# Kernel tuning notes

Measured on AMD Instinct MI355X. Metric: run time of the kernel, lower is better.

Reference implementation:

```python
import jax, jax.numpy as jnp
import numpy as np

B, N, CTX, IMG_DIM = 8, 256, 196, 1024
DIM, NUM_TOKENS, DEPTH = 512, 10000, 6
D_STATE, D_CONV, HEADS = 16, 4, 8
D_INNER = 2 * DIM
DT_RANK = DIM // 16  # mamba-ssm default ceil(d_model/16)
HEAD_DIM = DIM // HEADS


def setup_inputs() -> dict:
    key = jax.random.key(0)
    ks = [jax.random.fold_in(key, i) for i in range(40)]
    it = iter(ks)
    def rn(shape, s=0.02):
        return jax.random.normal(next(it), shape, dtype=jnp.float32) * s
    inp = {}
    inp["text"] = jax.random.randint(next(it), (B, N), 0, NUM_TOKENS)
    inp["images"] = jax.random.normal(next(it), (B, CTX, IMG_DIM), dtype=jnp.float32)
    inp["dyt_alpha"] = jnp.float32(0.5)
    inp["dyt_gamma"] = jnp.ones((IMG_DIM,), jnp.float32)
    inp["dyt_beta"] = jnp.zeros((IMG_DIM,), jnp.float32)
    inp["img_W"] = rn((IMG_DIM, DIM))
    inp["img_b"] = jnp.zeros((DIM,), jnp.float32)
    inp["gate1_W"] = rn((DIM, DIM // 4))
    inp["gate1_b"] = jnp.zeros((DIM // 4,), jnp.float32)
    inp["gate2_W"] = rn((DIM // 4, DIM))
    inp["gate2_b"] = jnp.zeros((DIM,), jnp.float32)
    inp["token_emb"] = rn((NUM_TOKENS, DIM), 0.01)
    inp["pos_emb"] = rn((1024, DIM))
    inp["ln1_g"] = jnp.ones((DEPTH, DIM), jnp.float32)
    inp["ln1_b"] = jnp.zeros((DEPTH, DIM), jnp.float32)
    inp["in_proj_W"] = rn((DEPTH, DIM, 2 * D_INNER))
    inp["conv_W"] = rn((DEPTH, D_INNER, D_CONV), 0.1)
    inp["conv_b"] = jnp.zeros((DEPTH, D_INNER), jnp.float32)
    inp["x_proj_W"] = rn((DEPTH, D_INNER, DT_RANK + 2 * D_STATE))
    inp["dt_proj_W"] = rn((DEPTH, DT_RANK, D_INNER), 0.1)
    inp["dt_proj_b"] = jnp.full((DEPTH, D_INNER), -4.0, jnp.float32)
    inp["A_log"] = jnp.tile(jnp.log(jnp.arange(1, D_STATE + 1, dtype=jnp.float32))[None, None, :], (DEPTH, D_INNER, 1))
    inp["D_skip"] = jnp.ones((DEPTH, D_INNER), jnp.float32)
    inp["out_proj_W"] = rn((DEPTH, D_INNER, DIM))
    inp["ln2_g"] = jnp.ones((DEPTH, DIM), jnp.float32)
    inp["ln2_b"] = jnp.zeros((DEPTH, DIM), jnp.float32)
    inp["attn_in_W"] = rn((DEPTH, 3 * DIM, DIM))
    inp["attn_in_b"] = jnp.zeros((DEPTH, 3 * DIM), jnp.float32)
    inp["attn_out_W"] = rn((DEPTH, DIM, DIM))
    inp["attn_out_b"] = jnp.zeros((DEPTH, DIM), jnp.float32)
    inp["fnorm_g"] = jnp.ones((DIM,), jnp.float32)
    inp["fnorm_b"] = jnp.zeros((DIM,), jnp.float32)
    inp["logits_W"] = rn((DIM, NUM_TOKENS), 0.01)
    inp["logits_b"] = jnp.zeros((NUM_TOKENS,), jnp.float32)
    return inp


def _layernorm(x, g, b, eps=1e-5):
    m = x.mean(-1, keepdims=True)
    v = ((x - m) ** 2).mean(-1, keepdims=True)
    return (x - m) * jax.lax.rsqrt(v + eps) * g + b


def _silu(x):
    return x * jax.nn.sigmoid(x)


def _mamba(x, inW, cW, cb, xpW, dtW, dtb, A_log, D_skip, outW):
    # x: [b, n, DIM] -> [b, n, DIM]; selective scan (S6)
    b, n, _ = x.shape
    xz = x @ inW                                  # [b,n,2*di]
    xi, z = jnp.split(xz, 2, axis=-1)
    # causal depthwise conv1d, kernel D_CONV
    xp = jnp.pad(xi, ((0, 0), (D_CONV - 1, 0), (0, 0)))
    xc = sum(xp[:, k:k + n, :] * cW[:, k] for k in range(D_CONV)) + cb
    xc = _silu(xc)                                # [b,n,di]
    dbl = xc @ xpW                                # [b,n,dt_rank+2*ds]
    dt = jax.nn.softplus(dbl[..., :DT_RANK] @ dtW + dtb)      # [b,n,di]
    Bm = dbl[..., DT_RANK:DT_RANK + D_STATE]      # [b,n,ds]
    Cm = dbl[..., DT_RANK + D_STATE:]             # [b,n,ds]
    A = -jnp.exp(A_log)                           # [di,ds]
    dA = jnp.exp(dt[..., None] * A)               # [b,n,di,ds]
    dBx = dt[..., None] * Bm[:, :, None, :] * xc[..., None]   # [b,n,di,ds]
    def step(h, inputs):
        dA_t, dBx_t, C_t = inputs
        h = h * dA_t + dBx_t                      # [b,di,ds]
        y = jnp.einsum('bds,bs->bd', h, C_t)
        return h, y
    h0 = jnp.zeros((b, D_INNER, D_STATE), x.dtype)
    _, ys = jax.lax.scan(step, h0, (dA.transpose(1, 0, 2, 3), dBx.transpose(1, 0, 2, 3), Cm.transpose(1, 0, 2)))
    y = ys.transpose(1, 0, 2) + xc * D_skip       # [b,n,di]
    y = y * _silu(z)
    return y @ outW


def _cross_attn(q_in, kv, inW, inb, outW, outb):
    # torch nn.MultiheadAttention (batch_first) with packed in_proj
    Wq, Wk, Wv = jnp.split(inW, 3, axis=0)
    bq, bk, bv = jnp.split(inb, 3)
    def heads(t):
        return t.reshape(t.shape[0], t.shape[1], HEADS, HEAD_DIM).transpose(0, 2, 1, 3)
    q = heads(q_in @ Wq.T + bq)
    k = heads(kv @ Wk.T + bk)
    v = heads(kv @ Wv.T + bv)
    scale = HEAD_DIM ** -0.5
    att = jax.nn.softmax(jnp.einsum('bhqd,bhkd->bhqk', q * scale, k), axis=-1)
    o = jnp.einsum('bhqk,bhkd->bhqd', att, v).transpose(0, 2, 1, 3)
    o = o.reshape(q_in.shape)
    return o @ outW.T + outb


def _forward(text, images, dyt_alpha, dyt_gamma, dyt_beta, img_W, img_b,
             gate1_W, gate1_b, gate2_W, gate2_b, token_emb, pos_emb,
             ln1_g, ln1_b, in_proj_W, conv_W, conv_b, x_proj_W, dt_proj_W,
             dt_proj_b, A_log, D_skip, out_proj_W, ln2_g, ln2_b,
             attn_in_W, attn_in_b, attn_out_W, attn_out_b,
             fnorm_g, fnorm_b, logits_W, logits_b):
    # img_proj: DyT -> Linear (dropout = identity at eval)
    img = dyt_gamma * jnp.tanh(dyt_alpha * images) + dyt_beta
    img = img @ img_W + img_b                     # [b,ctx,dim]
    # MedicalAttentionGate: mean-pool over sequence -> channel gate
    att = img.mean(axis=1)                        # [b,dim]
    att = jax.nn.gelu(att @ gate1_W + gate1_b, approximate=False)
    att = jax.nn.sigmoid(att @ gate2_W + gate2_b)
    img = img * att[:, None, :]
    # decoder
    n = text.shape[1]
    x = token_emb[text] + pos_emb[:n]
    for l in range(DEPTH):
        xn = _layernorm(x, ln1_g[l], ln1_b[l])
        x = x + _mamba(xn, in_proj_W[l], conv_W[l], conv_b[l], x_proj_W[l],
                       dt_proj_W[l], dt_proj_b[l], A_log[l], D_skip[l], out_proj_W[l])
        xn = _layernorm(x, ln2_g[l], ln2_b[l])
        x = x + _cross_attn(xn, img, attn_in_W[l], attn_in_b[l], attn_out_W[l], attn_out_b[l])
    x = _layernorm(x, fnorm_g, fnorm_b)
    return x @ logits_W + logits_b                # [b,n,num_tokens]


def reference(text, images, dyt_alpha, dyt_gamma, dyt_beta, img_W, img_b,
              gate1_W, gate1_b, gate2_W, gate2_b, token_emb, pos_emb,
              ln1_g, ln1_b, in_proj_W, conv_W, conv_b, x_proj_W, dt_proj_W,
              dt_proj_b, A_log, D_skip, out_proj_W, ln2_g, ln2_b,
              attn_in_W, attn_in_b, attn_out_W, attn_out_b,
              fnorm_g, fnorm_b, logits_W, logits_b):
    return _forward(text, images, dyt_alpha, dyt_gamma, dyt_beta, img_W, img_b,
                    gate1_W, gate1_b, gate2_W, gate2_b, token_emb, pos_emb,
                    ln1_g, ln1_b, in_proj_W, conv_W, conv_b, x_proj_W, dt_proj_W,
                    dt_proj_b, A_log, D_skip, out_proj_W, ln2_g, ln2_b,
                    attn_in_W, attn_in_b, attn_out_W, attn_out_b,
                    fnorm_g, fnorm_b, logits_W, logits_b)
```

## Files before the change

kernel.cpp:

```cpp
#include <hip/hip_runtime.h>
#include <hip/hip_bf16.h>
#include <stdint.h>

#define B_    8
#define N_    256
#define CTX_  196
#define CTXP_ 224
#define CTXF_ 13
#define IMGD_ 1024
#define DIM_  512
#define DEPTH_ 6
#define DIN_  1024
#define DTR_  32
#define DST_  16
#define HEADS_ 8
#define HD_   64
#define NCHUNK_ 16
#define CLEN_   16
#define DG_     4

typedef __bf16 bf16x8 __attribute__((ext_vector_type(8)));
typedef __bf16 bf16x4 __attribute__((ext_vector_type(4)));
typedef float  f32x4  __attribute__((ext_vector_type(4)));

__device__ __forceinline__ float dpp_red16(float v) {
    int y;
    y = __builtin_amdgcn_update_dpp(0, __float_as_int(v), 0xB1, 0xF, 0xF, true);
    v += __int_as_float(y);
    y = __builtin_amdgcn_update_dpp(0, __float_as_int(v), 0x4E, 0xF, 0xF, true);
    v += __int_as_float(y);
    y = __builtin_amdgcn_update_dpp(0, __float_as_int(v), 0x141, 0xF, 0xF, true);
    v += __int_as_float(y);
    y = __builtin_amdgcn_update_dpp(0, __float_as_int(v), 0x140, 0xF, 0xF, true);
    v += __int_as_float(y);
    return v;
}
__device__ __forceinline__ float dpp_max16(float v) {
    int y;
    y = __builtin_amdgcn_update_dpp(0, __float_as_int(v), 0xB1, 0xF, 0xF, true);
    v = fmaxf(v, __int_as_float(y));
    y = __builtin_amdgcn_update_dpp(0, __float_as_int(v), 0x4E, 0xF, 0xF, true);
    v = fmaxf(v, __int_as_float(y));
    y = __builtin_amdgcn_update_dpp(0, __float_as_int(v), 0x141, 0xF, 0xF, true);
    v = fmaxf(v, __int_as_float(y));
    y = __builtin_amdgcn_update_dpp(0, __float_as_int(v), 0x140, 0xF, 0xF, true);
    v = fmaxf(v, __int_as_float(y));
    return v;
}

__device__ __forceinline__ void gload16(const void* g, void* l) {
    __builtin_amdgcn_global_load_lds(
        (const __attribute__((address_space(1))) uint32_t*)g,
        (__attribute__((address_space(3))) uint32_t*)l, 16, 0, 0);
}


__global__ void dyt_kernel(const float* __restrict__ img, const float* __restrict__ alpha_p,
                           const float* __restrict__ gamma, const float* __restrict__ beta,
                           __bf16* __restrict__ out, int total) {
    int i = blockIdx.x * 256 + threadIdx.x;
    if (i >= total) return;
    float a = alpha_p[0];
    int c = i & (IMGD_ - 1);
    out[i] = (__bf16)(gamma[c] * tanhf(a * img[i]) + beta[c]);
}

__global__ void pool_kernel(const float* __restrict__ imgf, float* __restrict__ pooled) {
    int i = blockIdx.x * 256 + threadIdx.x;
    if (i >= B_ * DIM_) return;
    int b = i >> 9, c = i & (DIM_ - 1);
    const float* p = imgf + (size_t)b * CTX_ * DIM_ + c;
    float s = 0.f;
    for (int t = 0; t < CTX_; ++t) s += p[t * DIM_];
    pooled[i] = s * (1.f / CTX_);
}

__global__ void gate1_kernel(const float* __restrict__ pooled, const float* __restrict__ W,
                             const float* __restrict__ bias, float* __restrict__ g1) {
    int i = blockIdx.x * 256 + threadIdx.x;
    if (i >= B_ * 128) return;
    int b = i >> 7, j = i & 127;
    const float* p = pooled + b * DIM_;
    float s = bias[j];
    for (int c = 0; c < DIM_; ++c) s += p[c] * W[c * 128 + j];
    g1[i] = 0.5f * s * (1.f + erff(s * 0.70710678118654752f));
}

__global__ void gate2_kernel(const float* __restrict__ g1, const float* __restrict__ W,
                             const float* __restrict__ bias, float* __restrict__ gate) {
    int i = blockIdx.x * 256 + threadIdx.x;
    if (i >= B_ * DIM_) return;
    int b = i >> 9, c = i & (DIM_ - 1);
    const float* p = g1 + b * 128;
    float s = bias[c];
    for (int j = 0; j < 128; ++j) s += p[j] * W[j * DIM_ + c];
    gate[i] = 1.f / (1.f + __expf(-s));
}

__global__ void scale_kernel(const float* __restrict__ imgf, const float* __restrict__ gate,
                             __bf16* __restrict__ imgfb) {
    int i = blockIdx.x * 256 + threadIdx.x;
    if (i >= B_ * CTX_ * DIM_) return;
    int c = i & (DIM_ - 1);
    int b = i / (CTX_ * DIM_);
    imgfb[i] = (__bf16)(imgf[i] * gate[b * DIM_ + c]);
}

__global__ void embed_kernel(const int* __restrict__ text, const float* __restrict__ temb,
                             const float* __restrict__ pemb, float* __restrict__ x) {
    int i = blockIdx.x * 256 + threadIdx.x;
    if (i >= B_ * N_ * DIM_) return;
    int c = i & (DIM_ - 1);
    int row = i >> 9;
    int n = row & (N_ - 1);
    int tok = text[row];
    x[i] = temb[(size_t)tok * DIM_ + c] + pemb[(size_t)n * DIM_ + c];
}

__global__ void ln_kernel(const float* __restrict__ x, const float* __restrict__ g,
                          const float* __restrict__ b, __bf16* __restrict__ o, int rows) {
    int row = blockIdx.x * 4 + (threadIdx.x >> 6);
    if (row >= rows) return;
    int lane = threadIdx.x & 63;
    const float* xr = x + (size_t)row * DIM_ + lane * 8;
    float4 v0 = ((const float4*)xr)[0];
    float4 v1 = ((const float4*)xr)[1];
    float r[8] = {v0.x, v0.y, v0.z, v0.w, v1.x, v1.y, v1.z, v1.w};
    float sum = 0.f, sq = 0.f;
    #pragma unroll
    for (int j = 0; j < 8; ++j) { sum += r[j]; sq += r[j] * r[j]; }
    #pragma unroll
    for (int m = 1; m < 64; m <<= 1) { sum += __shfl_xor(sum, m); sq += __shfl_xor(sq, m); }
    float mean = sum * (1.f / DIM_);
    float var  = sq * (1.f / DIM_) - mean * mean;
    float inv  = rsqrtf(fmaxf(var, 0.f) + 1e-5f);
    const float* gp = g + lane * 8;
    const float* bp = b + lane * 8;
    __bf16* op = o + (size_t)row * DIM_ + lane * 8;
    bf16x8 ov;
    #pragma unroll
    for (int j = 0; j < 8; ++j) ov[j] = (__bf16)((r[j] - mean) * inv * gp[j] + bp[j]);
    *(bf16x8*)op = ov;
}

__global__ void conv_silu_kernel(const __bf16* __restrict__ xzb, const float* __restrict__ cw,
                                 const float* __restrict__ cb, __bf16* __restrict__ xcb) {
    int idx = blockIdx.x * 256 + threadIdx.x;
    if (idx >= B_ * N_ * DIN_ / 4) return;
    int i4 = idx * 4;
    int d = i4 & (DIN_ - 1);
    int row = i4 >> 10;
    int n = row & (N_ - 1);
    int rowb = row - n;
    float4 acc = *(const float4*)(cb + d);
    #pragma unroll
    for (int k = 0; k < 4; ++k) {
        int m = n - 3 + k;
        if (m >= 0) {
            bf16x4 v = *(const bf16x4*)(xzb + (size_t)(rowb + m) * (2 * DIN_) + d);
            acc.x += (float)v[0] * cw[(d + 0) * 4 + k];
            acc.y += (float)v[1] * cw[(d + 1) * 4 + k];
            acc.z += (float)v[2] * cw[(d + 2) * 4 + k];
            acc.w += (float)v[3] * cw[(d + 3) * 4 + k];
        }
    }
    bf16x4 p;
    p[0] = (__bf16)(acc.x / (1.f + __expf(-acc.x)));
    p[1] = (__bf16)(acc.y / (1.f + __expf(-acc.y)));
    p[2] = (__bf16)(acc.z / (1.f + __expf(-acc.z)));
    p[3] = (__bf16)(acc.w / (1.f + __expf(-acc.w)));
    *(bf16x4*)(xcb + i4) = p;
}

__global__ void cvt_bf16_kernel(const float* __restrict__ src, __bf16* __restrict__ dst, int count) {
    int i = (blockIdx.x * 256 + threadIdx.x) * 4;
    if (i >= count) return;
    float4 v = *(const float4*)(src + i);
    bf16x4 p = {(__bf16)v.x, (__bf16)v.y, (__bf16)v.z, (__bf16)v.w};
    *(bf16x4*)(dst + i) = p;
}

__global__ void cvt_rows_kernel(const float* __restrict__ src, __bf16* __restrict__ dst,
                                int totalRows, int rpl, int off) {
    int t = blockIdx.x * 256 + threadIdx.x;
    int total = totalRows * (DIM_ / 4);
    if (t >= total) return;
    int i = t / (DIM_ / 4), c4 = (t % (DIM_ / 4)) * 4;
    int l = i / rpl, r = i % rpl;
    const float* s = src + ((size_t)l * 1536 + off + r) * DIM_ + c4;
    float4 v = *(const float4*)s;
    bf16x4 p = {(__bf16)v.x, (__bf16)v.y, (__bf16)v.z, (__bf16)v.w};
    *(bf16x4*)(dst + (size_t)i * DIM_ + c4) = p;
}

__global__ __launch_bounds__(256) void scanf_kernel(
    const __bf16* __restrict__ xcb, const float* __restrict__ dbl,
    const __bf16* __restrict__ xzb, const float* __restrict__ dtw,
    const float* __restrict__ dtb, const float* __restrict__ A_log,
    const float* __restrict__ Dsk, __bf16* __restrict__ ybb) {
    __shared__ float sdt[DG_][N_], su[DG_][N_];
    __shared__ float sA[DG_][256], sB[DG_][256];
    int bid = blockIdx.x;
    int nwg = gridDim.x;
    int bd = (bid & 7) * (nwg >> 3) + (bid >> 3);
    int dg = bd & (DIN_ / DG_ - 1), b = bd / (DIN_ / DG_);
    int d0 = dg * DG_;
    int tid = threadIdx.x, s = tid & 15, c = tid >> 4;
    {
        int row = b * N_ + tid;
        const float* dp = dbl + row * 64;
        float4 acc = *(const float4*)(dtb + d0);
        #pragma unroll
        for (int k = 0; k < DTR_; k += 4) {
            float4 dv = *(const float4*)(dp + k);
            float4 w0 = *(const float4*)(dtw + (k + 0) * DIN_ + d0);
            float4 w1 = *(const float4*)(dtw + (k + 1) * DIN_ + d0);
            float4 w2 = *(const float4*)(dtw + (k + 2) * DIN_ + d0);
            float4 w3 = *(const float4*)(dtw + (k + 3) * DIN_ + d0);
            acc.x += dv.x * w0.x + dv.y * w1.x + dv.z * w2.x + dv.w * w3.x;
            acc.y += dv.x * w0.y + dv.y * w1.y + dv.z * w2.y + dv.w * w3.y;
            acc.z += dv.x * w0.z + dv.y * w1.z + dv.z * w2.z + dv.w * w3.z;
            acc.w += dv.x * w0.w + dv.y * w1.w + dv.z * w2.w + dv.w * w3.w;
        }
        bf16x4 xcv4 = *(const bf16x4*)(xcb + (size_t)row * DIN_ + d0);
        float av[4] = {acc.x, acc.y, acc.z, acc.w};
        float xv[4] = {(float)xcv4[0], (float)xcv4[1], (float)xcv4[2], (float)xcv4[3]};
        #pragma unroll
        for (int g = 0; g < DG_; ++g) {
            float dt = fmaxf(av[g], 0.f) + __logf(1.f + __expf(-fabsf(av[g])));
            sdt[g][tid] = dt;
            su[g][tid] = dt * xv[g];
        }
    }
    float As4[DG_];
    #pragma unroll
    for (int g = 0; g < DG_; ++g) As4[g] = -__expf(A_log[((d0 + g) << 4) | s]);
    __syncthreads();
    int r0 = c * CLEN_;
    int row0 = b * N_ + r0;
    float a[DG_], hb[DG_];
    #pragma unroll
    for (int g = 0; g < DG_; ++g) { a[g] = 1.f; hb[g] = 0.f; }
    #pragma unroll 2
    for (int n = 0; n < CLEN_; ++n) {
        float Bv = dbl[(row0 + n) * 64 + 32 + s];
        #pragma unroll
        for (int g = 0; g < DG_; ++g) {
            float dA = __expf(sdt[g][r0 + n] * As4[g]);
            hb[g] = hb[g] * dA + su[g][r0 + n] * Bv;
            a[g] *= dA;
        }
    }
    #pragma unroll
    for (int g = 0; g < DG_; ++g) { sA[g][tid] = a[g]; sB[g][tid] = hb[g]; }
    __syncthreads();
    float h[DG_];
    #pragma unroll
    for (int g = 0; g < DG_; ++g) h[g] = 0.f;
    for (int j = 0; j < c; ++j)
        #pragma unroll
        for (int g = 0; g < DG_; ++g)
            h[g] = h[g] * sA[g][j * 16 + s] + sB[g][j * 16 + s];
    float4 Dv4 = *(const float4*)(Dsk + d0);
    float Dv[4] = {Dv4.x, Dv4.y, Dv4.z, Dv4.w};
    #pragma unroll 2
    for (int n = 0; n < CLEN_; ++n) {
        int row = row0 + n;
        float Bv = dbl[row * 64 + 32 + s];
        float Cv = dbl[row * 64 + 48 + s];
        float p[DG_];
        #pragma unroll
        for (int g = 0; g < DG_; ++g) {
            float dA = __expf(sdt[g][r0 + n] * As4[g]);
            h[g] = h[g] * dA + su[g][r0 + n] * Bv;
            p[g] = dpp_red16(h[g] * Cv);
        }
        if (s == 0) {
            bf16x4 xcv4 = *(const bf16x4*)(xcb + (size_t)row * DIN_ + d0);
            bf16x4 zz4  = *(const bf16x4*)(xzb + (size_t)row * (2 * DIN_) + DIN_ + d0);
            bf16x4 yo;
            #pragma unroll
            for (int g = 0; g < DG_; ++g) {
                float xv = (float)xcv4[g];
                float zv = (float)zz4[g];
                float y = (p[g] + xv * Dv[g]) * (zv / (1.f + __expf(-zv)));
                yo[g] = (__bf16)y;
            }
            *(bf16x4*)(ybb + (size_t)row * DIN_ + d0) = yo;
        }
    }
}


__global__ void tconv_kernel(const float* __restrict__ src, __bf16* __restrict__ dst,
                             int K, int N) {
    __shared__ float tile[32][33];
    int n0 = blockIdx.x * 32, k0 = blockIdx.y * 32;
    src += (size_t)blockIdx.z * K * N;
    dst += (size_t)blockIdx.z * K * N;
    int tx = threadIdx.x & 31, ty = threadIdx.x >> 5;
    #pragma unroll
    for (int i = 0; i < 32; i += 8) {
        int k = k0 + ty + i, n = n0 + tx;
        tile[ty + i][tx] = (k < K && n < N) ? src[(size_t)k * N + n] : 0.f;
    }
    __syncthreads();
    #pragma unroll
    for (int i = 0; i < 32; i += 8) {
        int n = n0 + ty + i, k = k0 + tx;
        if (n < N && k < K) dst[(size_t)n * K + k] = (__bf16)tile[tx][ty + i];
    }
}


template <int BM, int BN, int MODE, bool CMAJ = false>
__global__ __launch_bounds__(256) void mgemm_k(
    const __bf16* __restrict__ A, const __bf16* __restrict__ Bw,
    const float* __restrict__ bias, const float* __restrict__ res,
    void* __restrict__ Cp, void* __restrict__ Cp2,
    int M, int N, int K, int lda, int ldc) {
    constexpr int UA = BM * 4;
    constexpr int UB = BN * 4;
    constexpr int FM = BM / 32, FN = BN / 32;
    constexpr int CPAD = BN + 4;
    constexpr int STAGE_B = (UA + UB) * 32;
    constexpr int CS_B    = (MODE == 0) ? (BM / 2) * CPAD * 4 : 0;
    constexpr int SMEM_B  = STAGE_B > CS_B ? STAGE_B : CS_B;
    __shared__ __align__(16) char smem[SMEM_B];
    __bf16* As = (__bf16*)smem;
    __bf16* Bs = (__bf16*)(smem + (size_t)UA * 32);
    int tid = threadIdx.x;
    int ntx = gridDim.x;
    int nwg = ntx * gridDim.y;
    int bid = blockIdx.y * ntx + blockIdx.x;
    if ((nwg & 7) == 0) bid = (bid & 7) * (nwg >> 3) + (bid >> 3);
    int row0, col0;
    if constexpr (CMAJ) {
        int nty = nwg / ntx;
        row0 = (bid % nty) * BM;
        col0 = (bid / nty) * BN;
    } else {
        row0 = (bid / ntx) * BM;
        col0 = (bid % ntx) * BN;
    }
    int wave = tid >> 6, lane = tid & 63;
    int wm = (wave >> 1) * (BM / 2), wn = (wave & 1) * (BN / 2);
    int fr = lane & 15, fk = lane >> 4;
    f32x4 acc[FM][FN] = {};

    auto stage = [&](int buf, int k0) {
        #pragma unroll
        for (int j = 0; j < (UA + 255) / 256; ++j) {
            int u = j * 256 + tid;
            if ((UA & 255) == 0 || u < UA) {
                int ks = u / BM, r = u % BM;
                gload16(A + (size_t)(row0 + r) * lda + k0 + ks * 8, &As[((size_t)buf * UA + u) * 8]);
            }
        }
        #pragma unroll
        for (int j = 0; j < (UB + 255) / 256; ++j) {
            int u = j * 256 + tid;
            if ((UB & 255) == 0 || u < UB) {
                int ks = u / BN, r = u % BN;
                gload16(Bw + (size_t)(col0 + r) * K + k0 + ks * 8, &Bs[((size_t)buf * UB + u) * 8]);
            }
        }
    };

    stage(0, 0);
    __syncthreads();
    int NK = K >> 5;
    for (int kt = 0; kt < NK; ++kt) {
        int cur = kt & 1;
        if (kt + 1 < NK) stage(cur ^ 1, (kt + 1) << 5);
        bf16x8 af[FM], bg[FN];
        #pragma unroll
        for (int mf = 0; mf < FM; ++mf)
            af[mf] = *(const bf16x8*)&As[((size_t)cur * UA + fk * BM + wm + mf * 16 + fr) * 8];
        #pragma unroll
        for (int nf = 0; nf < FN; ++nf)
            bg[nf] = *(const bf16x8*)&Bs[((size_t)cur * UB + fk * BN + wn + nf * 16 + fr) * 8];
        #pragma unroll
        for (int mf = 0; mf < FM; ++mf)
            #pragma unroll
            for (int nf = 0; nf < FN; ++nf)
                acc[mf][nf] = __builtin_amdgcn_mfma_f32_16x16x32_bf16(af[mf], bg[nf], acc[mf][nf], 0, 0, 0);
        __syncthreads();
    }
    if constexpr (MODE == 0) {
        float* Cs = (float*)smem;
        #pragma unroll
        for (int half = 0; half < 2; ++half) {
            if (wm == half * (BM / 2)) {
                #pragma unroll
                for (int mf = 0; mf < FM; ++mf)
                    #pragma unroll
                    for (int nf = 0; nf < FN; ++nf)
                        #pragma unroll
                        for (int e = 0; e < 4; ++e)
                            Cs[(mf * 16 + fk * 4 + e) * CPAD + wn + nf * 16 + fr] = acc[mf][nf][e];
            }
            __syncthreads();
            for (int u = tid; u < (BM / 2) * BN / 4; u += 256) {
                int r = u / (BN / 4), c4 = (u % (BN / 4)) * 4;
                int gm = row0 + half * (BM / 2) + r, gn = col0 + c4;
                if (gm < M && gn < N) {
                    f32x4 v = *(const f32x4*)&Cs[r * CPAD + c4];
                    if (bias) v += *(const f32x4*)(bias + gn);
                    size_t idx = (size_t)gm * ldc + gn;
                    if (res) v += *(const f32x4*)(res + idx);
                    *(f32x4*)((float*)Cp + idx) = v;
                }
            }
            __syncthreads();
        }
    } else {
        #pragma unroll
        for (int mf = 0; mf < FM; ++mf) {
            #pragma unroll
            for (int nf = 0; nf < FN; ++nf) {
                int gn = col0 + wn + nf * 16 + fr;
                if (gn >= N) continue;
                float bb = (MODE != 3 && bias) ? bias[gn] : 0.f;
                #pragma unroll
                for (int e = 0; e < 4; ++e) {
                    int gm = row0 + wm + mf * 16 + fk * 4 + e;
                    if (gm >= M) continue;
                    float v = acc[mf][nf][e] + bb;
                    if constexpr (MODE == 1) {
                        ((__bf16*)Cp)[(size_t)gm * ldc + gn] = (__bf16)v;
                    } else {
                        int l = gn >> 10, j = gn & 1023;
                        float vb = v + res[l * 1536 + 512 + j];
                        if (j < DIM_) {
                            ((__bf16*)Cp)[(size_t)l * (B_ * CTX_) * DIM_ + (size_t)gm * DIM_ + j] = (__bf16)vb;
                        } else {
                            int jj = j - DIM_;
                            int bimg = gm / CTX_, k = gm - bimg * CTX_;
                            ((__bf16*)Cp2)[(((size_t)l * B_ * HEADS_ + bimg * HEADS_ + (jj >> 6)) * HD_ + (jj & 63)) * CTXP_ + k] = (__bf16)vb;
                        }
                    }
                }
            }
        }
    }
}

template <int BM, int BN, int MODE = 0, bool CMAJ = false>
static inline void mgemm(const __bf16* A, const __bf16* Bw, const float* bias,
                         const float* res, void* C, void* C2, int M, int N, int K,
                         int lda, int ldc, hipStream_t s) {
    dim3 g((N + BN - 1) / BN, (M + BM - 1) / BM);
    mgemm_k<BM, BN, MODE, CMAJ><<<g, 256, 0, s>>>(A, Bw, bias, res, C, C2, M, N, K, lda, ldc);
}

#define KP_ 72
#define PP_ 232

__global__ __launch_bounds__(256) void attn_k(
    const __bf16* __restrict__ qb, const __bf16* __restrict__ kbb,
    const __bf16* __restrict__ vbT, __bf16* __restrict__ obb) {
    __shared__ __align__(16) __bf16 Ks[CTXP_ * KP_];
    __shared__ __align__(16) __bf16 Ps[64 * PP_];
    int z = blockIdx.z, b = z >> 3, h = z & 7;
    int tid = threadIdx.x, wave = tid >> 6, lane = tid & 63;
    int fr = lane & 15, fk = lane >> 4;
    int q0 = blockIdx.y * 64;
    #pragma unroll
    for (int i = 0; i < 7; ++i) {
        int idx = i * 256 + tid;
        int r = idx >> 3, cu = (idx & 7) * 8;
        uint4 v = {0u, 0u, 0u, 0u};
        if (r < CTX_) v = *(const uint4*)(kbb + ((size_t)(b * CTX_ + r)) * DIM_ + h * HD_ + cu);
        *(uint4*)&Ks[r * KP_ + cu] = v;
    }
    bf16x8 aq[2];
    {
        int qrow = b * N_ + q0 + wave * 16 + fr;
        #pragma unroll
        for (int t = 0; t < 2; ++t)
            aq[t] = *(const bf16x8*)(qb + (size_t)qrow * DIM_ + h * HD_ + t * 32 + fk * 8);
    }
    __syncthreads();
    f32x4 acc[CTXF_] = {};
    #pragma unroll
    for (int t = 0; t < 2; ++t)
        #pragma unroll
        for (int cb = 0; cb < CTXF_; ++cb) {
            bf16x8 bg = *(const bf16x8*)&Ks[(cb * 16 + fr) * KP_ + t * 32 + fk * 8];
            acc[cb] = __builtin_amdgcn_mfma_f32_16x16x32_bf16(aq[t], bg, acc[cb], 0, 0, 0);
        }
    #pragma unroll
    for (int e = 0; e < 4; ++e) {
        float m = -1e30f;
        #pragma unroll
        for (int cb = 0; cb < CTXF_; ++cb) {
            float sv = acc[cb][e] * 0.125f;
            if (cb * 16 + fr >= CTX_) sv = -1e30f;
            acc[cb][e] = sv;
            m = fmaxf(m, sv);
        }
        m = dpp_max16(m);
        float ssum = 0.f;
        #pragma unroll
        for (int cb = 0; cb < CTXF_; ++cb) {
            float p = __expf(acc[cb][e] - m);
            acc[cb][e] = p;
            ssum += p;
        }
        ssum = dpp_red16(ssum);
        float inv = 1.f / ssum;
        #pragma unroll
        for (int cb = 0; cb < CTXF_; ++cb)
            Ps[(wave * 16 + fk * 4 + e) * PP_ + cb * 16 + fr] = (__bf16)(acc[cb][e] * inv);
        Ps[(wave * 16 + fk * 4 + e) * PP_ + 208 + fr] = (__bf16)0.f;
    }
    __syncthreads();
    f32x4 acc2[4] = {};
    const __bf16* vB = vbT + (size_t)z * HD_ * CTXP_;
    #pragma unroll
    for (int sl = 0; sl < 7; ++sl) {
        bf16x8 ap = *(const bf16x8*)&Ps[(wave * 16 + fr) * PP_ + sl * 32 + fk * 8];
        #pragma unroll
        for (int nf = 0; nf < 4; ++nf) {
            bf16x8 bv = *(const bf16x8*)(vB + (size_t)(nf * 16 + fr) * CTXP_ + sl * 32 + fk * 8);
            acc2[nf] = __builtin_amdgcn_mfma_f32_16x16x32_bf16(ap, bv, acc2[nf], 0, 0, 0);
        }
    }
    #pragma unroll
    for (int nf = 0; nf < 4; ++nf)
        #pragma unroll
        for (int e = 0; e < 4; ++e) {
            int gm = b * N_ + q0 + wave * 16 + fk * 4 + e;
            obb[(size_t)gm * DIM_ + h * HD_ + nf * 16 + fr] = (__bf16)acc2[nf][e];
        }
}


extern "C" void kernel_launch(void* const* d_in, const int* in_sizes, int n_in,
                              void* d_out, int out_size, void* d_ws, size_t ws_size,
                              hipStream_t stream) {
    const int*   text   = (const int*)d_in[0];
    const float* images = (const float*)d_in[1];
    const float* alphap = (const float*)d_in[2];
    const float* dgam   = (const float*)d_in[3];
    const float* dbeta  = (const float*)d_in[4];
    const float* imgW   = (const float*)d_in[5];
    const float* imgb   = (const float*)d_in[6];
    const float* g1W    = (const float*)d_in[7];
    const float* g1b    = (const float*)d_in[8];
    const float* g2W    = (const float*)d_in[9];
    const float* g2b    = (const float*)d_in[10];
    const float* temb   = (const float*)d_in[11];
    const float* pemb   = (const float*)d_in[12];
    const float* ln1g   = (const float*)d_in[13];
    const float* ln1b   = (const float*)d_in[14];
    const float* inW    = (const float*)d_in[15];
    const float* convW  = (const float*)d_in[16];
    const float* convb  = (const float*)d_in[17];
    const float* xpW    = (const float*)d_in[18];
    const float* dtW    = (const float*)d_in[19];
    const float* dtb    = (const float*)d_in[20];
    const float* Alog   = (const float*)d_in[21];
    const float* Dsk    = (const float*)d_in[22];
    const float* outW   = (const float*)d_in[23];
    const float* ln2g   = (const float*)d_in[24];
    const float* ln2b   = (const float*)d_in[25];
    const float* ainW   = (const float*)d_in[26];
    const float* ainb   = (const float*)d_in[27];
    const float* aoutW  = (const float*)d_in[28];
    const float* aoutb  = (const float*)d_in[29];
    const float* fng    = (const float*)d_in[30];
    const float* fnb    = (const float*)d_in[31];
    const float* lgW    = (const float*)d_in[32];
    const float* lgb    = (const float*)d_in[33];
    float* out = (float*)d_out;

    float* w = (float*)d_ws;
    float* imgd   = w; w += (size_t)B_ * CTX_ * IMGD_;
    float* imgf   = w; w += (size_t)B_ * CTX_ * DIM_;
    float* pooled = w; w += B_ * DIM_;
    float* g1     = w; w += B_ * 128;
    float* gate   = w; w += B_ * DIM_;
    float* x      = w; w += (size_t)B_ * N_ * DIM_;
    float* xn     = w; w += (size_t)B_ * N_ * DIM_;
    float* dblb   = w; w += (size_t)B_ * N_ * 64;
    __bf16* xzb   = (__bf16*)w; w += (size_t)B_ * N_ * 2 * DIN_ / 2;
    __bf16* xcb   = (__bf16*)w; w += (size_t)B_ * N_ * DIN_ / 2;
    __bf16* imgfb = (__bf16*)w; w += (size_t)B_ * CTX_ * DIM_ / 2;
    __bf16* ybb   = (__bf16*)w; w += (size_t)B_ * N_ * DIN_ / 2;
    __bf16* qb    = (__bf16*)w; w += (size_t)B_ * N_ * DIM_ / 2;
    __bf16* kbb   = (__bf16*)w; w += (size_t)DEPTH_ * B_ * CTX_ * DIM_ / 2;
    __bf16* vbT   = (__bf16*)w; w += (size_t)DEPTH_ * B_ * HEADS_ * HD_ * CTXP_ / 2;
    __bf16* obb   = (__bf16*)w; w += (size_t)B_ * N_ * DIM_ / 2;
    __bf16* lgT   = (__bf16*)w; w += (size_t)10000 * DIM_ / 2;
    __bf16* inpT  = (__bf16*)w; w += (size_t)DEPTH_ * 2 * DIN_ * DIM_ / 2;
    __bf16* outpT = (__bf16*)w; w += (size_t)DEPTH_ * DIM_ * DIN_ / 2;
    __bf16* qWB   = (__bf16*)w; w += (size_t)DEPTH_ * DIM_ * DIM_ / 2;
    __bf16* kvWB  = (__bf16*)w; w += (size_t)DEPTH_ * 2 * DIM_ * DIM_ / 2;
    __bf16* aoutB = (__bf16*)w; w += (size_t)DEPTH_ * DIM_ * DIM_ / 2;
    __bf16* imgWT = (__bf16*)w; w += (size_t)DIM_ * IMGD_ / 2;
    __bf16* xpWT  = (__bf16*)w; w += (size_t)DEPTH_ * 64 * DIN_ / 2;
    __bf16* imgdb = (__bf16*)imgd;
    __bf16* xnb   = (__bf16*)xn;

    const int TOKENS = B_ * N_;
    const int IMGT   = B_ * CTX_;

    hipMemsetAsync(vbT, 0, (size_t)DEPTH_ * B_ * HEADS_ * HD_ * CTXP_ * sizeof(__bf16), stream);

    tconv_kernel<<<dim3(2 * DIN_ / 32, DIM_ / 32, DEPTH_), 256, 0, stream>>>(inW,  inpT,  DIM_, 2 * DIN_);
    tconv_kernel<<<dim3(DIM_ / 32, DIN_ / 32, DEPTH_),     256, 0, stream>>>(outW, outpT, DIN_, DIM_);
    tconv_kernel<<<dim3(DIM_ / 32, IMGD_ / 32, 1),         256, 0, stream>>>(imgW, imgWT, IMGD_, DIM_);
    tconv_kernel<<<dim3(64 / 32, DIN_ / 32, DEPTH_),       256, 0, stream>>>(xpW,  xpWT,  DIN_, 64);
    tconv_kernel<<<dim3((10000 + 31) / 32, DIM_ / 32, 1),  256, 0, stream>>>(lgW, lgT, DIM_, 10000);
    cvt_rows_kernel<<<(DEPTH_ * DIM_ * (DIM_ / 4) + 255) / 256, 256, 0, stream>>>(
        ainW, qWB, DEPTH_ * DIM_, DIM_, 0);
    cvt_rows_kernel<<<(DEPTH_ * 2 * DIM_ * (DIM_ / 4) + 255) / 256, 256, 0, stream>>>(
        ainW, kvWB, DEPTH_ * 2 * DIM_, 2 * DIM_, DIM_);
    cvt_bf16_kernel<<<(DEPTH_ * DIM_ * DIM_ / 4 + 255) / 256, 256, 0, stream>>>(aoutW, aoutB, DEPTH_ * DIM_ * DIM_);

    {
        int total = B_ * CTX_ * IMGD_;
        dyt_kernel<<<(total + 255) / 256, 256, 0, stream>>>(images, alphap, dgam, dbeta, imgdb, total);
        mgemm<32, 64>(imgdb, imgWT, imgb, nullptr, imgf, nullptr, IMGT, DIM_, IMGD_, IMGD_, DIM_, stream);
        pool_kernel<<<(B_ * DIM_ + 255) / 256, 256, 0, stream>>>(imgf, pooled);
        gate1_kernel<<<(B_ * 128 + 255) / 256, 256, 0, stream>>>(pooled, g1W, g1b, g1);
        gate2_kernel<<<(B_ * DIM_ + 255) / 256, 256, 0, stream>>>(g1, g2W, g2b, gate);
        scale_kernel<<<(B_ * CTX_ * DIM_ + 255) / 256, 256, 0, stream>>>(imgf, gate, imgfb);
    }
    embed_kernel<<<(TOKENS * DIM_ + 255) / 256, 256, 0, stream>>>(text, temb, pemb, x);

    mgemm<64, 128, 3, true>(imgfb, kvWB, nullptr, ainb, kbb, vbT,
                            IMGT, DEPTH_ * 2 * DIM_, DIM_, DIM_, 0, stream);

    for (int l = 0; l < DEPTH_; ++l) {
        const __bf16* inpT_l  = inpT  + (size_t)l * 2 * DIN_ * DIM_;
        const __bf16* outpT_l = outpT + (size_t)l * DIM_ * DIN_;
        const __bf16* qWB_l   = qWB   + (size_t)l * DIM_ * DIM_;
        const __bf16* aoutB_l = aoutB + (size_t)l * DIM_ * DIM_;
        const __bf16* xpWT_l  = xpWT  + (size_t)l * 64 * DIN_;
        const __bf16* kbb_l   = kbb   + (size_t)l * IMGT * DIM_;
        const __bf16* vbT_l   = vbT   + (size_t)l * B_ * HEADS_ * HD_ * CTXP_;
        const float* cw    = convW + (size_t)l * DIN_ * 4;
        const float* cb    = convb + (size_t)l * DIN_;
        const float* dtw   = dtW  + (size_t)l * DTR_ * DIN_;
        const float* dtbi  = dtb  + (size_t)l * DIN_;
        const float* alog  = Alog + (size_t)l * DIN_ * DST_;
        const float* dsk   = Dsk  + (size_t)l * DIN_;
        const float* ab    = ainb + (size_t)l * 3 * DIM_;
        const float* aob   = aoutb + (size_t)l * DIM_;

        ln_kernel<<<TOKENS / 4, 256, 0, stream>>>(x, ln1g + l * DIM_, ln1b + l * DIM_, xnb, TOKENS);
        mgemm<64, 128, 1>(xnb, inpT_l, nullptr, nullptr, xzb, nullptr, TOKENS, 2 * DIN_, DIM_, DIM_, 2 * DIN_, stream);
        conv_silu_kernel<<<(TOKENS * DIN_ / 4 + 255) / 256, 256, 0, stream>>>(xzb, cw, cb, xcb);
        mgemm<32, 64>(xcb, xpWT_l, nullptr, nullptr, dblb, nullptr, TOKENS, 64, DIN_, DIN_, 64, stream);
        scanf_kernel<<<B_ * DIN_ / DG_, 256, 0, stream>>>(xcb, dblb, xzb, dtw, dtbi, alog, dsk, ybb);
        mgemm<32, 64>(ybb, outpT_l, nullptr, x, x, nullptr, TOKENS, DIM_, DIN_, DIN_, DIM_, stream);

        ln_kernel<<<TOKENS / 4, 256, 0, stream>>>(x, ln2g + l * DIM_, ln2b + l * DIM_, xnb, TOKENS);
        mgemm<32, 64, 1>(xnb, qWB_l, ab, nullptr, qb, nullptr, TOKENS, DIM_, DIM_, DIM_, DIM_, stream);
        attn_k<<<dim3(1, 4, B_ * HEADS_), 256, 0, stream>>>(qb, kbb_l, vbT_l, obb);
        mgemm<32, 64>(obb, aoutB_l, aob, x, x, nullptr, TOKENS, DIM_, DIM_, DIM_, DIM_, stream);
    }

    ln_kernel<<<TOKENS / 4, 256, 0, stream>>>(x, fng, fnb, xnb, TOKENS);
    mgemm<128, 128, 0, true>(xnb, lgT, lgb, nullptr, out, nullptr, TOKENS, 10000, DIM_, DIM_, 10000, stream);
}
```

Baseline: 1.127 ms.

## Add triple-buffered LDS pipeline with vmcnt waits to large GEMMs

Adds an optional three-stage shared-memory pipeline to the MFMA GEMM. It prefetches two K-tiles ahead and uses explicit s_waitcnt vmcnt counts and raw s_barrier in place of a full __syncthreads, so global-to-LDS loads overlap more MFMA work. The path is enabled for the KV projection, the in_proj GEMM and the logits GEMM. It uses more LDS per block, which may cut occupancy, and correctness depends on the hand-counted vmcnt values matching the loads issued per thread.

```diff
diff --git a/kernel.cpp b/kernel.cpp
--- a/kernel.cpp
+++ b/kernel.cpp
@@ -313,7 +313,7 @@
 }
 
 
-template <int BM, int BN, int MODE, bool CMAJ = false>
+template <int BM, int BN, int MODE, bool CMAJ = false, bool PIPE3 = false>
 __global__ __launch_bounds__(256) void mgemm_k(
     const __bf16* __restrict__ A, const __bf16* __restrict__ Bw,
     const float* __restrict__ bias, const float* __restrict__ res,
@@ -322,13 +322,16 @@
     constexpr int UA = BM * 4;
     constexpr int UB = BN * 4;
     constexpr int FM = BM / 32, FN = BN / 32;
+    constexpr int NBUF = PIPE3 ? 3 : 2;
+    constexpr int LPT = UA / 256 + UB / 256;
+    static_assert(!PIPE3 || (UA % 256 == 0 && UB % 256 == 0), "PIPE3 needs uniform loads");
     constexpr int CPAD = BN + 4;
-    constexpr int STAGE_B = (UA + UB) * 32;
+    constexpr int STAGE_B = NBUF * (UA + UB) * 16;
     constexpr int CS_B    = (MODE == 0) ? (BM / 2) * CPAD * 4 : 0;
     constexpr int SMEM_B  = STAGE_B > CS_B ? STAGE_B : CS_B;
     __shared__ __align__(16) char smem[SMEM_B];
     __bf16* As = (__bf16*)smem;
-    __bf16* Bs = (__bf16*)(smem + (size_t)UA * 32);
+    __bf16* Bs = (__bf16*)(smem + (size_t)NBUF * UA * 16);
     int tid = threadIdx.x;
     int ntx = gridDim.x;
     int nwg = ntx * gridDim.y;
@@ -366,13 +369,7 @@
             }
         }
     };
-
-    stage(0, 0);
-    __syncthreads();
-    int NK = K >> 5;
-    for (int kt = 0; kt < NK; ++kt) {
-        int cur = kt & 1;
-        if (kt + 1 < NK) stage(cur ^ 1, (kt + 1) << 5);
+    auto mfma_step = [&](int cur) {
         bf16x8 af[FM], bg[FN];
         #pragma unroll
         for (int mf = 0; mf < FM; ++mf)
@@ -385,7 +382,33 @@
             #pragma unroll
             for (int nf = 0; nf < FN; ++nf)
                 acc[mf][nf] = __builtin_amdgcn_mfma_f32_16x16x32_bf16(af[mf], bg[nf], acc[mf][nf], 0, 0, 0);
+    };
+
+    int NK = K >> 5;
+    if constexpr (PIPE3) {
+        stage(0, 0);
+        if (NK > 1) stage(1, 32);
+        for (int kt = 0; kt < NK; ++kt) {
+            if (kt + 1 < NK) {
+                if constexpr (LPT == 3) asm volatile("s_waitcnt vmcnt(3)" ::: "memory");
+                else                    asm volatile("s_waitcnt vmcnt(4)" ::: "memory");
+            } else {
+                asm volatile("s_waitcnt vmcnt(0)" ::: "memory");
+            }
+            asm volatile("s_barrier" ::: "memory");
+            mfma_step(kt % 3);
+            asm volatile("s_barrier" ::: "memory");
+            if (kt + 2 < NK) stage((kt + 2) % 3, (kt + 2) << 5);
+        }
+    } else {
+        stage(0, 0);
         __syncthreads();
+        for (int kt = 0; kt < NK; ++kt) {
+            int cur = kt & 1;
+            if (kt + 1 < NK) stage(cur ^ 1, (kt + 1) << 5);
+            mfma_step(cur);
+            __syncthreads();
+        }
     }
     if constexpr (MODE == 0) {
         float* Cs = (float*)smem;
@@ -446,12 +469,12 @@
     }
 }
 
-template <int BM, int BN, int MODE = 0, bool CMAJ = false>
+template <int BM, int BN, int MODE = 0, bool CMAJ = false, bool PIPE3 = false>
 static inline void mgemm(const __bf16* A, const __bf16* Bw, const float* bias,
                          const float* res, void* C, void* C2, int M, int N, int K,
                          int lda, int ldc, hipStream_t s) {
     dim3 g((N + BN - 1) / BN, (M + BM - 1) / BM);
-    mgemm_k<BM, BN, MODE, CMAJ><<<g, 256, 0, s>>>(A, Bw, bias, res, C, C2, M, N, K, lda, ldc);
+    mgemm_k<BM, BN, MODE, CMAJ, PIPE3><<<g, 256, 0, s>>>(A, Bw, bias, res, C, C2, M, N, K, lda, ldc);
 }
 
 #define KP_ 72
@@ -631,8 +654,8 @@
     }
     embed_kernel<<<(TOKENS * DIM_ + 255) / 256, 256, 0, stream>>>(text, temb, pemb, x);
 
-    mgemm<64, 128, 3, true>(imgfb, kvWB, nullptr, ainb, kbb, vbT,
-                            IMGT, DEPTH_ * 2 * DIM_, DIM_, DIM_, 0, stream);
+    mgemm<64, 128, 3, true, true>(imgfb, kvWB, nullptr, ainb, kbb, vbT,
+                                  IMGT, DEPTH_ * 2 * DIM_, DIM_, DIM_, 0, stream);
 
     for (int l = 0; l < DEPTH_; ++l) {
         const __bf16* inpT_l  = inpT  + (size_t)l * 2 * DIN_ * DIM_;
@@ -652,7 +675,7 @@
         const float* aob   = aoutb + (size_t)l * DIM_;
 
         ln_kernel<<<TOKENS / 4, 256, 0, stream>>>(x, ln1g + l * DIM_, ln1b + l * DIM_, xnb, TOKENS);
-        mgemm<64, 128, 1>(xnb, inpT_l, nullptr, nullptr, xzb, nullptr, TOKENS, 2 * DIN_, DIM_, DIM_, 2 * DIN_, stream);
+        mgemm<64, 128, 1, false, true>(xnb, inpT_l, nullptr, nullptr, xzb, nullptr, TOKENS, 2 * DIN_, DIM_, DIM_, 2 * DIN_, stream);
         conv_silu_kernel<<<(TOKENS * DIN_ / 4 + 255) / 256, 256, 0, stream>>>(xzb, cw, cb, xcb);
         mgemm<32, 64>(xcb, xpWT_l, nullptr, nullptr, dblb, nullptr, TOKENS, 64, DIN_, DIN_, 64, stream);
         scanf_kernel<<<B_ * DIN_ / DG_, 256, 0, stream>>>(xcb, dblb, xzb, dtw, dtbi, alog, dsk, ybb);
@@ -665,5 +688,5 @@
     }
 
     ln_kernel<<<TOKENS / 4, 256, 0, stream>>>(x, fng, fnb, xnb, TOKENS);
-    mgemm<128, 128, 0, true>(xnb, lgT, lgb, nullptr, out, nullptr, TOKENS, 10000, DIM_, DIM_, 10000, stream);
-}
+    mgemm<128, 128, 0, true, true>(xnb, lgT, lgb, nullptr, out, nullptr, TOKENS, 10000, DIM_, DIM_, 10000, stream);
+}
```

New measurement: 1.123 ms. No clear change (-0.3%).
